# Kernel tuning notes

Hardware: AMD Instinct MI355X
Metric: run time of the kernel (lower is better)

Reference implementation:

```python
import jax, jax.numpy as jnp
import numpy as np


def setup_inputs() -> dict:
    key = jax.random.key(0)
    k1, k2 = jax.random.split(key)
    B, N, M, D = 32, 1024, 1024, 256
    h1 = jax.random.normal(k1, (B, N, D), dtype=jnp.float32)
    h2 = jax.random.normal(k2, (B, M, D), dtype=jnp.float32)
    return {"h1": h1, "h2": h2}


def reference(h1, h2):
    # Soft Hausdorff over B graph pairs.
    # torch cdist with p=2 here is sum_d |x-y|^2 == squared L2 distance;
    N = h1.shape[1]
    M = h2.shape[1]
    sq1 = jnp.sum(h1 * h1, axis=-1)  # [B, N]
    sq2 = jnp.sum(h2 * h2, axis=-1)  # [B, M]
    cross = jnp.einsum('bnd,bmd->bnm', h1, h2)  # [B, N, M]
    dist = sq1[:, :, None] + sq2[:, None, :] - 2.0 * cross
    dist = jnp.maximum(dist, 0.0)  # guard tiny negative fp noise
    a = jnp.min(dist, axis=1).sum(axis=-1)  # min over N for each col, then sum over M
    b = jnp.min(dist, axis=2).sum(axis=-1)  # min over M for each row, then sum over N
    return (a + b) / min(N, M)  # [B]
```

## Files before the change

### kernel.cpp

```cpp
#include <hip/hip_runtime.h>
#include <hip/hip_bf16.h>
#include <stdint.h>

#define BB 32
#define NN 1024
#define MM 1024
#define DD 256

typedef __attribute__((ext_vector_type(8))) short short8;
typedef __attribute__((ext_vector_type(4))) float floatx4;

__device__ inline unsigned short f2bf(float x) {
    union { __hip_bfloat16 h; unsigned short u; } cv;
    cv.h = __float2bfloat16(x);
    return cv.u;
}
__device__ inline short8 pack8(float4 a, float4 b) {
    short8 o;
    o[0] = f2bf(a.x); o[1] = f2bf(a.y); o[2] = f2bf(a.z); o[3] = f2bf(a.w);
    o[4] = f2bf(b.x); o[5] = f2bf(b.y); o[6] = f2bf(b.z); o[7] = f2bf(b.w);
    return o;
}
__device__ inline void async_copy16(void* lds, const void* g) {
    __builtin_amdgcn_global_load_lds(
        (const __attribute__((address_space(1))) unsigned int*)g,
        (__attribute__((address_space(3))) unsigned int*)lds, 16, 0, 0);
}
__device__ inline void async_copy4(void* lds, const void* g) {
    __builtin_amdgcn_global_load_lds(
        (const __attribute__((address_space(1))) unsigned int*)g,
        (__attribute__((address_space(3))) unsigned int*)lds, 4, 0, 0);
}

__global__ __launch_bounds__(256) void convert_kernel(
        const float* __restrict__ h2, unsigned short* __restrict__ h2b,
        float* __restrict__ sq2, unsigned int* __restrict__ minb) {
    int g = blockIdx.x * 256 + threadIdx.x;
    if (g < 2 * BB * NN) minb[g] = 0x7F800000u;

    int wid  = blockIdx.x * 4 + (threadIdx.x >> 6);
    int lane = threadIdx.x & 63;
    int l5   = lane & 31;
    int row  = wid * 2 + (lane >> 5);

    const float4* p = (const float4*)(h2 + (size_t)row * DD) + l5 * 2;
    float4 a = p[0], c = p[1];

    float s = a.x*a.x + a.y*a.y + a.z*a.z + a.w*a.w
            + c.x*c.x + c.y*c.y + c.z*c.z + c.w*c.w;
    #pragma unroll
    for (int off = 16; off; off >>= 1) s += __shfl_xor(s, off, 64);

    *(short8*)((char*)(h2b + (size_t)row * DD) + l5 * 16) = pack8(a, c);
    if (l5 == 0) sq2[row] = s;
}

__global__ __launch_bounds__(512, 2) void gemm_kernel(
        const float* __restrict__ h1, const unsigned short* __restrict__ h2b,
        const float* __restrict__ sq2,
        unsigned int* __restrict__ rowmin, unsigned int* __restrict__ colmin) {
    __shared__ __align__(16) char pool[131072];
    #define PANEL (pool + 65536)
    __shared__ __align__(16) float  sq1_s[128];
    __shared__ __align__(16) float  sq2_s[1024];
    __shared__ unsigned int cl_s[1024];

    const int b    = blockIdx.x;
    const int tile = blockIdx.y;
    const int n0   = tile * 128;

    const int tid  = threadIdx.x;
    const int wave = tid >> 6;
    const int lane = tid & 63;
    const int wn   = (wave >> 2) * 64;
    const int wm   = (wave & 3) * 32;

    const char* Ag = (const char*)(h1 + ((size_t)b * NN + n0) * DD);
    const char* Bg = (const char*)(h2b + (size_t)b * MM * DD);

    const int krow = lane >> 4;
    const int rrow = lane & 15;
    const int rx   = rrow & 7;
    const int lrow = krow * 4;
    const int lcol = rrow;

    cl_s[tid] = 0x7F800000u; cl_s[tid + 512] = 0x7F800000u;

    #pragma unroll
    for (int t = 0; t < 2; ++t)
        async_copy4((char*)sq2_s + t * 2048 + wave * 256,
                    (const char*)(sq2 + b * MM) + t * 2048 + wave * 256 + lane * 4);

    #pragma unroll 1
    for (int q = 0; q < 4; ++q) {
        #pragma unroll
        for (int t = 0; t < 4; ++t) {
            int rl_ = t * 8 + wave;
            async_copy16(pool + rl_ * 1024,
                Ag + (size_t)(q * 32 + rl_) * 1024 + ((lane ^ (rl_ & 7)) << 4));
        }
        asm volatile("s_waitcnt vmcnt(0) lgkmcnt(0)" ::: "memory");
        __builtin_amdgcn_s_barrier();
        __builtin_amdgcn_sched_barrier(0);

        {
            int prow = tid >> 4;
            int s_   = lane & 15;
            int rg   = q * 32 + prow;
            const char* rp = pool + prow * 1024;
            float sum = 0.f;
            #pragma unroll
            for (int jj = 0; jj < 2; ++jj) {
                int g0 = s_ * 4 + jj * 2;
                float4 f0 = *(const float4*)(rp + ((g0 ^ (prow & 7)) << 4));
                float4 f1 = *(const float4*)(rp + (((g0 + 1) ^ (prow & 7)) << 4));
                sum += f0.x*f0.x + f0.y*f0.y + f0.z*f0.z + f0.w*f0.w
                     + f1.x*f1.x + f1.y*f1.y + f1.z*f1.z + f1.w*f1.w;
                int ub = s_ * 2 + jj;
                *(short8*)(PANEL + (size_t)rg * 512 + ((ub ^ (prow & 7)) << 4))
                    = pack8(f0, f1);
            }
            sum += __shfl_xor(sum, 1, 64);
            sum += __shfl_xor(sum, 2, 64);
            sum += __shfl_xor(sum, 4, 64);
            sum += __shfl_xor(sum, 8, 64);
            if (s_ == 0) sq1_s[rg] = sum;
        }
        asm volatile("s_waitcnt lgkmcnt(0)" ::: "memory");
        __builtin_amdgcn_sched_barrier(0);
        __builtin_amdgcn_s_barrier();
        __builtin_amdgcn_sched_barrier(0);
    }

    short8 af[4][8];
    #pragma unroll
    for (int i = 0; i < 4; ++i) {
        #pragma unroll
        for (int kq = 0; kq < 8; ++kq) {
            int r = wn + i * 16 + rrow;
            int g = kq * 4 + krow;
            af[i][kq] = *(const short8*)(PANEL + (size_t)r * 512 + ((g ^ rx) << 4));
        }
    }
    asm volatile("s_waitcnt lgkmcnt(0)" ::: "memory");
    __builtin_amdgcn_sched_barrier(0);
    __builtin_amdgcn_s_barrier();
    __builtin_amdgcn_sched_barrier(0);

    const int br = lane >> 4;
    const int bp = lane & 15;
    #define STAGE(s_)                                                         \
        { int mt_ = (s_) >> 1, h_ = (s_) & 1;                                 \
          char* bb_ = pool + ((s_) & 3) * 32768;                              \
          _Pragma("unroll")                                                   \
          for (int c = 0; c < 4; ++c) {                                       \
            int ch_ = wave * 4 + c;                                           \
            int r_  = ch_ * 4 + br;                                           \
            async_copy16(bb_ + ch_ * 1024,                                    \
                Bg + (size_t)(mt_ * 128 + r_) * 512 + h_ * 256                \
                   + ((bp ^ (r_ & 7)) << 4)); } }

    STAGE(0); STAGE(1); STAGE(2);

    float rmin[4][4];
    #pragma unroll
    for (int i = 0; i < 4; ++i)
        #pragma unroll
        for (int r = 0; r < 4; ++r) rmin[i][r] = 3.0e38f;

    #pragma unroll 1
    for (int mt = 0; mt < 8; ++mt) {
        floatx4 acc[4][2] = {};

        #pragma unroll
        for (int h = 0; h < 2; ++h) {
            const int s = mt * 2 + h;
            if (s < 14)      { asm volatile("s_waitcnt vmcnt(8)" ::: "memory"); }
            else if (s < 15) { asm volatile("s_waitcnt vmcnt(4)" ::: "memory"); }
            else             { asm volatile("s_waitcnt vmcnt(0)" ::: "memory"); }
            __builtin_amdgcn_s_barrier();
            __builtin_amdgcn_sched_barrier(0);

            if (s < 13) STAGE(s + 3);

            const char* Bb = pool + (s & 3) * 32768;
            __builtin_amdgcn_s_setprio(1);
            #pragma unroll
            for (int kk = 0; kk < 4; ++kk) {
                short8 bfv[2];
                #pragma unroll
                for (int j = 0; j < 2; ++j) {
                    int g = kk * 4 + krow;
                    bfv[j] = *(const short8*)(Bb
                             + (size_t)(wm + j * 16 + rrow) * 256 + ((g ^ rx) << 4));
                }
                #pragma unroll
                for (int i = 0; i < 4; ++i)
                    #pragma unroll
                    for (int j = 0; j < 2; ++j)
                        acc[i][j] = __builtin_amdgcn_mfma_f32_16x16x32_bf16(
                            af[i][h * 4 + kk], bfv[j], acc[i][j], 0, 0, 0);
            }
            __builtin_amdgcn_s_setprio(0);
        }

        float s2v0 = sq2_s[mt * 128 + wm + lcol];
        float s2v1 = sq2_s[mt * 128 + wm + 16 + lcol];

        float cmin0 = 3.0e38f, cmin1 = 3.0e38f;
        #pragma unroll
        for (int i = 0; i < 4; ++i) {
            float4 s1q = *(const float4*)(&sq1_s[wn + i * 16 + lrow]);
            #pragma unroll
            for (int r = 0; r < 4; ++r) {
                float s1x = ((const float*)&s1q)[r];
                float d0 = fmaxf(s1x + s2v0 - 2.0f * acc[i][0][r], 0.0f);
                float d1 = fmaxf(s1x + s2v1 - 2.0f * acc[i][1][r], 0.0f);
                rmin[i][r] = fminf(rmin[i][r], fminf(d0, d1));
                cmin0 = fminf(cmin0, d0);
                cmin1 = fminf(cmin1, d1);
            }
        }
        cmin0 = fminf(cmin0, __shfl_xor(cmin0, 16, 64));
        cmin0 = fminf(cmin0, __shfl_xor(cmin0, 32, 64));
        cmin1 = fminf(cmin1, __shfl_xor(cmin1, 16, 64));
        cmin1 = fminf(cmin1, __shfl_xor(cmin1, 32, 64));
        if (lane < 16) {
            atomicMin(&cl_s[mt * 128 + wm + lcol],      __float_as_uint(cmin0));
            atomicMin(&cl_s[mt * 128 + wm + 16 + lcol], __float_as_uint(cmin1));
        }
    }

    unsigned int* rm = rowmin + b * NN + n0;
    #pragma unroll
    for (int i = 0; i < 4; ++i) {
        #pragma unroll
        for (int r = 0; r < 4; ++r) {
            float v = rmin[i][r];
            #pragma unroll
            for (int off = 1; off < 16; off <<= 1)
                v = fminf(v, __shfl_xor(v, off, 64));
            if (lcol == 0)
                atomicMin(&rm[wn + i * 16 + lrow + r], __float_as_uint(v));
        }
    }

    __syncthreads();
    unsigned int* cmg = colmin + b * MM;
    atomicMin(&cmg[tid],       cl_s[tid]);
    atomicMin(&cmg[tid + 512], cl_s[tid + 512]);
    #undef STAGE
    #undef PANEL
}

__global__ __launch_bounds__(256) void finalize_kernel(
        const unsigned int* __restrict__ rowmin,
        const unsigned int* __restrict__ colmin,
        float* __restrict__ out) {
    int b = blockIdx.x;
    int tid = threadIdx.x;
    float s = 0.0f;
    for (int i = tid; i < NN; i += 256) s += __uint_as_float(rowmin[b * NN + i]);
    for (int i = tid; i < MM; i += 256) s += __uint_as_float(colmin[b * MM + i]);
    #pragma unroll
    for (int off = 32; off; off >>= 1) s += __shfl_xor(s, off, 64);
    __shared__ float wsum[4];
    if ((tid & 63) == 0) wsum[tid >> 6] = s;
    __syncthreads();
    if (tid == 0) out[b] = (wsum[0] + wsum[1] + wsum[2] + wsum[3]) * (1.0f / 1024.0f);
}

extern "C" void kernel_launch(void* const* d_in, const int* in_sizes, int n_in,
                              void* d_out, int out_size, void* d_ws, size_t ws_size,
                              hipStream_t stream) {
    const float* h1 = (const float*)d_in[0];
    const float* h2 = (const float*)d_in[1];
    float* out = (float*)d_out;

    char* ws = (char*)d_ws;
    unsigned short* h2b = (unsigned short*)ws;
    float* sq2          = (float*)(ws + (size_t)BB * MM * DD * 2);
    unsigned int* rowmin = (unsigned int*)(sq2 + BB * MM);
    unsigned int* colmin = rowmin + BB * NN;

    hipLaunchKernelGGL(convert_kernel, dim3(4096), dim3(256), 0, stream,
                       h2, h2b, sq2, rowmin);

    hipLaunchKernelGGL(gemm_kernel, dim3(BB, 8), dim3(512), 0, stream,
                       h1, h2b, sq2, rowmin, colmin);

    hipLaunchKernelGGL(finalize_kernel, dim3(BB), dim3(256), 0, stream,
                       rowmin, colmin, out);
}
```

Before: 49.13 us.

## Stream A from LDS per k-step, widen M tile, double-buffer A and B staging

```diff
diff --git a/kernel.cpp b/kernel.cpp
--- a/kernel.cpp
+++ b/kernel.cpp
@@ -60,10 +60,12 @@
         const float* __restrict__ sq2,
         unsigned int* __restrict__ rowmin, unsigned int* __restrict__ colmin) {
     __shared__ __align__(16) char pool[131072];
-    #define PANEL (pool + 65536)
+    #define PANEL (pool)
+    #define STG(h_) (pool + 65536 + (h_) * 32768)
     __shared__ __align__(16) float  sq1_s[128];
     __shared__ __align__(16) float  sq2_s[1024];
     __shared__ unsigned int cl_s[1024];
+    __shared__ unsigned int rl_s[128];
 
     const int b    = blockIdx.x;
     const int tile = blockIdx.y;
@@ -73,7 +75,7 @@
     const int wave = tid >> 6;
     const int lane = tid & 63;
     const int wn   = (wave >> 2) * 64;
-    const int wm   = (wave & 3) * 32;
+    const int wm   = (wave & 3) * 64;
 
     const char* Ag = (const char*)(h1 + ((size_t)b * NN + n0) * DD);
     const char* Bg = (const char*)(h2b + (size_t)b * MM * DD);
@@ -85,21 +87,27 @@
     const int lcol = rrow;
 
     cl_s[tid] = 0x7F800000u; cl_s[tid + 512] = 0x7F800000u;
+    if (tid < 128) rl_s[tid] = 0x7F800000u;
 
     #pragma unroll
     for (int t = 0; t < 2; ++t)
         async_copy4((char*)sq2_s + t * 2048 + wave * 256,
                     (const char*)(sq2 + b * MM) + t * 2048 + wave * 256 + lane * 4);
 
+    #define STAGE_A(q_)                                                       \
+        { _Pragma("unroll")                                                   \
+          for (int t = 0; t < 4; ++t) {                                       \
+            int rl_ = t * 8 + wave;                                           \
+            async_copy16(STG((q_) & 1) + rl_ * 1024,                          \
+                Ag + (size_t)((q_) * 32 + rl_) * 1024                         \
+                   + ((lane ^ (rl_ & 7)) << 4)); } }
+
+    STAGE_A(0);
     #pragma unroll 1
     for (int q = 0; q < 4; ++q) {
-        #pragma unroll
-        for (int t = 0; t < 4; ++t) {
-            int rl_ = t * 8 + wave;
-            async_copy16(pool + rl_ * 1024,
-                Ag + (size_t)(q * 32 + rl_) * 1024 + ((lane ^ (rl_ & 7)) << 4));
-        }
-        asm volatile("s_waitcnt vmcnt(0) lgkmcnt(0)" ::: "memory");
+        if (q < 3) STAGE_A(q + 1);
+        if (q < 3) { asm volatile("s_waitcnt vmcnt(4)" ::: "memory"); }
+        else       { asm volatile("s_waitcnt vmcnt(0)" ::: "memory"); }
         __builtin_amdgcn_s_barrier();
         __builtin_amdgcn_sched_barrier(0);
 
@@ -107,7 +115,7 @@
             int prow = tid >> 4;
             int s_   = lane & 15;
             int rg   = q * 32 + prow;
-            const char* rp = pool + prow * 1024;
+            const char* rp = STG(q & 1) + prow * 1024;
             float sum = 0.f;
             #pragma unroll
             for (int jj = 0; jj < 2; ++jj) {
@@ -132,35 +140,20 @@
         __builtin_amdgcn_sched_barrier(0);
     }
 
-    short8 af[4][8];
-    #pragma unroll
-    for (int i = 0; i < 4; ++i) {
-        #pragma unroll
-        for (int kq = 0; kq < 8; ++kq) {
-            int r = wn + i * 16 + rrow;
-            int g = kq * 4 + krow;
-            af[i][kq] = *(const short8*)(PANEL + (size_t)r * 512 + ((g ^ rx) << 4));
-        }
-    }
-    asm volatile("s_waitcnt lgkmcnt(0)" ::: "memory");
-    __builtin_amdgcn_sched_barrier(0);
-    __builtin_amdgcn_s_barrier();
-    __builtin_amdgcn_sched_barrier(0);
-
-    const int br = lane >> 4;
-    const int bp = lane & 15;
-    #define STAGE(s_)                                                         \
-        { int mt_ = (s_) >> 1, h_ = (s_) & 1;                                 \
-          char* bb_ = pool + ((s_) & 3) * 32768;                              \
+    const int rl  = lane >> 3;
+    const int bcu = (lane & 7) ^ rl;
+    #define STAGE_B(s_)                                                       \
+        { int mt_ = (s_) >> 2, ks_ = (s_) & 3;                                \
+          char* bb_ = STG((s_) & 1);                                          \
           _Pragma("unroll")                                                   \
           for (int c = 0; c < 4; ++c) {                                       \
             int ch_ = wave * 4 + c;                                           \
-            int r_  = ch_ * 4 + br;                                           \
+            int r_  = ch_ * 8 + rl;                                           \
             async_copy16(bb_ + ch_ * 1024,                                    \
-                Bg + (size_t)(mt_ * 128 + r_) * 512 + h_ * 256                \
-                   + ((bp ^ (r_ & 7)) << 4)); } }
-
-    STAGE(0); STAGE(1); STAGE(2);
+                Bg + (size_t)(mt_ * 256 + r_) * 512 + ks_ * 128               \
+                   + (bcu << 4)); } }
+
+    STAGE_B(0); STAGE_B(1);
 
     float rmin[4][4];
     #pragma unroll
@@ -169,69 +162,82 @@
         for (int r = 0; r < 4; ++r) rmin[i][r] = 3.0e38f;
 
     #pragma unroll 1
-    for (int mt = 0; mt < 8; ++mt) {
-        floatx4 acc[4][2] = {};
-
-        #pragma unroll
-        for (int h = 0; h < 2; ++h) {
-            const int s = mt * 2 + h;
-            if (s < 14)      { asm volatile("s_waitcnt vmcnt(8)" ::: "memory"); }
-            else if (s < 15) { asm volatile("s_waitcnt vmcnt(4)" ::: "memory"); }
-            else             { asm volatile("s_waitcnt vmcnt(0)" ::: "memory"); }
+    for (int mt = 0; mt < 4; ++mt) {
+        floatx4 acc[4][4] = {};
+
+        #pragma unroll
+        for (int ks = 0; ks < 4; ++ks) {
+            const int s = mt * 4 + ks;
+            if (s < 15) { asm volatile("s_waitcnt vmcnt(4)" ::: "memory"); }
+            else        { asm volatile("s_waitcnt vmcnt(0)" ::: "memory"); }
             __builtin_amdgcn_s_barrier();
             __builtin_amdgcn_sched_barrier(0);
 
-            if (s < 13) STAGE(s + 3);
-
-            const char* Bb = pool + (s & 3) * 32768;
+            const char* Bb = STG(s & 1);
             __builtin_amdgcn_s_setprio(1);
             #pragma unroll
-            for (int kk = 0; kk < 4; ++kk) {
-                short8 bfv[2];
+            for (int kk = 0; kk < 2; ++kk) {
+                short8 af_t[4], bfv[4];
                 #pragma unroll
-                for (int j = 0; j < 2; ++j) {
+                for (int i = 0; i < 4; ++i) {
+                    int g = (ks * 2 + kk) * 4 + krow;
+                    af_t[i] = *(const short8*)(PANEL
+                        + (size_t)(wn + i * 16 + rrow) * 512 + ((g ^ rx) << 4));
+                }
+                #pragma unroll
+                for (int j = 0; j < 4; ++j) {
                     int g = kk * 4 + krow;
                     bfv[j] = *(const short8*)(Bb
-                             + (size_t)(wm + j * 16 + rrow) * 256 + ((g ^ rx) << 4));
+                        + (size_t)(wm + j * 16 + rrow) * 128 + ((g ^ rx) << 4));
                 }
                 #pragma unroll
                 for (int i = 0; i < 4; ++i)
                     #pragma unroll
-                    for (int j = 0; j < 2; ++j)
+                    for (int j = 0; j < 4; ++j)
                         acc[i][j] = __builtin_amdgcn_mfma_f32_16x16x32_bf16(
-                            af[i][h * 4 + kk], bfv[j], acc[i][j], 0, 0, 0);
+                            af_t[i], bfv[j], acc[i][j], 0, 0, 0);
             }
             __builtin_amdgcn_s_setprio(0);
-        }
-
-        float s2v0 = sq2_s[mt * 128 + wm + lcol];
-        float s2v1 = sq2_s[mt * 128 + wm + 16 + lcol];
-
-        float cmin0 = 3.0e38f, cmin1 = 3.0e38f;
+
+            asm volatile("s_waitcnt lgkmcnt(0)" ::: "memory");
+            __builtin_amdgcn_sched_barrier(0);
+            __builtin_amdgcn_s_barrier();
+            if (s < 14) STAGE_B(s + 2);
+        }
+
+        float s2v[4];
+        #pragma unroll
+        for (int j = 0; j < 4; ++j)
+            s2v[j] = sq2_s[mt * 256 + wm + j * 16 + lcol];
+
+        float cmin[4] = {3.0e38f, 3.0e38f, 3.0e38f, 3.0e38f};
         #pragma unroll
         for (int i = 0; i < 4; ++i) {
             float4 s1q = *(const float4*)(&sq1_s[wn + i * 16 + lrow]);
             #pragma unroll
             for (int r = 0; r < 4; ++r) {
                 float s1x = ((const float*)&s1q)[r];
-                float d0 = fmaxf(s1x + s2v0 - 2.0f * acc[i][0][r], 0.0f);
-                float d1 = fmaxf(s1x + s2v1 - 2.0f * acc[i][1][r], 0.0f);
-                rmin[i][r] = fminf(rmin[i][r], fminf(d0, d1));
-                cmin0 = fminf(cmin0, d0);
-                cmin1 = fminf(cmin1, d1);
+                float pm = 3.0e38f;
+                #pragma unroll
+                for (int j = 0; j < 4; ++j) {
+                    float d = fmaxf(s1x + s2v[j] - 2.0f * acc[i][j][r], 0.0f);
+                    pm = fminf(pm, d);
+                    cmin[j] = fminf(cmin[j], d);
+                }
+                rmin[i][r] = fminf(rmin[i][r], pm);
             }
         }
-        cmin0 = fminf(cmin0, __shfl_xor(cmin0, 16, 64));
-        cmin0 = fminf(cmin0, __shfl_xor(cmin0, 32, 64));
-        cmin1 = fminf(cmin1, __shfl_xor(cmin1, 16, 64));
-        cmin1 = fminf(cmin1, __shfl_xor(cmin1, 32, 64));
-        if (lane < 16) {
-            atomicMin(&cl_s[mt * 128 + wm + lcol],      __float_as_uint(cmin0));
-            atomicMin(&cl_s[mt * 128 + wm + 16 + lcol], __float_as_uint(cmin1));
+        #pragma unroll
+        for (int j = 0; j < 4; ++j) {
+            float c = cmin[j];
+            c = fminf(c, __shfl_xor(c, 16, 64));
+            c = fminf(c, __shfl_xor(c, 32, 64));
+            if (lane < 16)
+                atomicMin(&cl_s[mt * 256 + wm + j * 16 + lcol],
+                          __float_as_uint(c));
         }
     }
 
-    unsigned int* rm = rowmin + b * NN + n0;
     #pragma unroll
     for (int i = 0; i < 4; ++i) {
         #pragma unroll
@@ -241,16 +247,19 @@
             for (int off = 1; off < 16; off <<= 1)
                 v = fminf(v, __shfl_xor(v, off, 64));
             if (lcol == 0)
-                atomicMin(&rm[wn + i * 16 + lrow + r], __float_as_uint(v));
+                atomicMin(&rl_s[wn + i * 16 + lrow + r], __float_as_uint(v));
         }
     }
-
     __syncthreads();
+
     unsigned int* cmg = colmin + b * MM;
     atomicMin(&cmg[tid],       cl_s[tid]);
     atomicMin(&cmg[tid + 512], cl_s[tid + 512]);
-    #undef STAGE
+    if (tid < 128) rowmin[b * NN + n0 + tid] = rl_s[tid];
+    #undef STAGE_A
+    #undef STAGE_B
     #undef PANEL
+    #undef STG
 }
 
 __global__ __launch_bounds__(256) void finalize_kernel(
```

After: 48.96 us. About the same (-0.4%).
